# Optimization experiments

Measured on AMD Instinct MI355X. Metric: run time of the kernel, lower is better.

## Reference

```python
import jax, jax.numpy as jnp
import numpy as np

DIM = 768
HEADS = 12
HEAD_DIM = DIM // HEADS
EPS_ATTN = 1e-6
LN_EPS = 1e-5


def _piece_weight():
    # BlockDistanceConv with num_patches_per_side=16, patch_group_size=16 -> 4x4 blocks
    bps = 4
    centers = np.array([[i + 0.5, j + 0.5] for i in range(bps) for j in range(bps)], dtype=np.float32)
    d = np.linalg.norm(centers[:, None, :] - centers[None, :, :], axis=-1)
    mat = np.cos(d / d.max() * np.pi / 4.0)  # 'cos' transform
    mat = mat / mat.sum(axis=0, keepdims=True)
    return jnp.asarray(mat, dtype=jnp.float32)  # [16, 16], out = W @ x over piece channels


def setup_inputs() -> dict:
    key = jax.random.key(0)
    ks = jax.random.split(key, 4)
    B, N, W, C = 128, 16, 16, DIM
    x = jax.random.normal(ks[0], (B, N, W, C), dtype=jnp.float32)
    ln_gamma = jnp.ones((C,), dtype=jnp.float32)
    ln_beta = jnp.zeros((C,), dtype=jnp.float32)
    w_qkv = jax.random.normal(ks[1], (C, 3 * C), dtype=jnp.float32) * (C ** -0.5)
    w_out = jax.random.normal(ks[2], (C, C), dtype=jnp.float32) * (C ** -0.5)
    b_out = jnp.zeros((C,), dtype=jnp.float32)
    w_piece = _piece_weight()
    return {"x": x, "ln_gamma": ln_gamma, "ln_beta": ln_beta, "w_qkv": w_qkv,
            "w_out": w_out, "b_out": b_out, "w_piece": w_piece}


def reference(x, ln_gamma, ln_beta, w_qkv, w_out, b_out, w_piece):
    B, N, W, C = x.shape
    H, D = HEADS, HEAD_DIM
    # LayerNorm over channel dim
    mu = jnp.mean(x, axis=-1, keepdims=True)
    var = jnp.mean((x - mu) ** 2, axis=-1, keepdims=True)
    xn = (x - mu) * jax.lax.rsqrt(var + LN_EPS) * ln_gamma + ln_beta
    # qkv projection (no bias)
    qkv = xn @ w_qkv  # [B,N,W,3C]
    q, k, v = jnp.split(qkv, 3, axis=-1)
    # relu kernel feature map
    q = jax.nn.relu(q) + EPS_ATTN
    k = jax.nn.relu(k) + EPS_ATTN
    # split heads: 'b n w (h d) -> b h n w d'
    def heads(t):
        return t.reshape(B, N, W, H, D).transpose(0, 3, 1, 2, 4)
    q, k, v = heads(q), heads(k), heads(v)
    # per-window kv = k^T v  (sum over window positions w)  -> [B,H,N,D,D]
    kv = jnp.einsum('bhnwd,bhnwe->bhnde', k, v)
    # BlockDistanceConv: 1x1 conv mixing over piece dim N with fixed weights
    kv = jnp.einsum('ij,bhjde->bhide', w_piece, kv)
    # out = q @ kv  -> [B,H,N,W,D]
    out = jnp.einsum('bhnwd,bhnde->bhnwe', q, kv)
    # merge heads: 'b h n w d -> b n w (h d)'
    out = out.transpose(0, 2, 3, 1, 4).reshape(B, N, W, H * D)
    # output projection (dropout is identity in eval)
    return out @ w_out + b_out
```

## Files before the change

### kernel.cpp

```cpp
#include <hip/hip_runtime.h>

#define DIM 768
#define HEADS 12
#define TOK 32768

typedef unsigned short ushort_t;
typedef __attribute__((ext_vector_type(8))) short short8v;
typedef __attribute__((ext_vector_type(4))) float f32x4;
typedef __attribute__((ext_vector_type(4))) unsigned short us4;

__device__ __forceinline__ ushort_t f2bf(float x) {
  union { float f; unsigned u; } c; c.f = x;
  unsigned r = (c.u + 0x7FFFu + ((c.u >> 16) & 1u)) >> 16;
  return (ushort_t)r;
}

__device__ __forceinline__ void gload_lds16(const void* g, void* l) {
  __builtin_amdgcn_global_load_lds((const __attribute__((address_space(1))) void*)g,
                                   (__attribute__((address_space(3))) void*)l, 16, 0, 0);
}

__global__ __launch_bounds__(256) void ln_kernel(const float* __restrict__ x,
                                                 const float* __restrict__ g,
                                                 const float* __restrict__ be,
                                                 ushort_t* __restrict__ xn) {
  int t = blockIdx.x;
  int tid = threadIdx.x;
  const float* row = x + (size_t)t * DIM;
  float v0 = row[tid], v1 = row[tid + 256], v2 = row[tid + 512];
  float s  = v0 + v1 + v2;
  float sq = v0 * v0 + v1 * v1 + v2 * v2;
  #pragma unroll
  for (int off = 32; off; off >>= 1) {
    s  += __shfl_down(s, off);
    sq += __shfl_down(sq, off);
  }
  __shared__ float ls[4], lq[4];
  int wid = tid >> 6, lane = tid & 63;
  if (lane == 0) { ls[wid] = s; lq[wid] = sq; }
  __syncthreads();
  s  = ls[0] + ls[1] + ls[2] + ls[3];
  sq = lq[0] + lq[1] + lq[2] + lq[3];
  float mu  = s * (1.0f / DIM);
  float var = sq * (1.0f / DIM) - mu * mu;
  float rs  = rsqrtf(var + 1e-5f);
  ushort_t* orow = xn + (size_t)t * DIM;
  orow[tid]       = f2bf((v0 - mu) * rs * g[tid]       + be[tid]);
  orow[tid + 256] = f2bf((v1 - mu) * rs * g[tid + 256] + be[tid + 256]);
  orow[tid + 512] = f2bf((v2 - mu) * rs * g[tid + 512] + be[tid + 512]);
}

__global__ __launch_bounds__(256) void convT(const float* __restrict__ src,
                                             ushort_t* __restrict__ dst, int R, int Ccol) {
  __shared__ float tile[32][33];
  int c0 = blockIdx.x * 32, r0 = blockIdx.y * 32;
  int tx = threadIdx.x & 31, ty = threadIdx.x >> 5;
  #pragma unroll
  for (int i = 0; i < 32; i += 8)
    tile[ty + i][tx] = src[(size_t)(r0 + ty + i) * Ccol + c0 + tx];
  __syncthreads();
  #pragma unroll
  for (int i = 0; i < 32; i += 8)
    dst[(size_t)(c0 + ty + i) * R + r0 + tx] = f2bf(tile[tx][ty + i]);
}

template <int MODE>
__global__ __launch_bounds__(256) void gemm_ring(const ushort_t* __restrict__ A,
                                                 const ushort_t* __restrict__ Bt,
                                                 ushort_t* __restrict__ qbf,
                                                 ushort_t* __restrict__ kbf,
                                                 ushort_t* __restrict__ vTbf,
                                                 const float* __restrict__ bias,
                                                 float* __restrict__ C) {
  const int K = DIM, Kb = DIM * 2;
  const int N = (MODE == 0) ? 3 * DIM : DIM;
  const int nbn = N / 128;
  const int NT = K / 32;
  __shared__ __align__(16) char lds[4 * 16384];

  int bid = blockIdx.x;
  int qd = gridDim.x >> 3;
  int wid = (bid & 7) * qd + (bid >> 3);
  int bm = wid / nbn, bn = wid % nbn;
  int row0 = bm * 128, col0 = bn * 128;
  int t = threadIdx.x;
  int lane = t & 63, wave = t >> 6;
  int wr = wave >> 1, wc = wave & 1;

  const char* Ag = (const char*)(A + (size_t)row0 * K);
  const char* Bg = (const char*)(Bt + (size_t)col0 * K);

  int o0 = t * 16;
  int o1 = 4096 + t * 16;
  int r0s = o0 >> 6, r1s = o1 >> 6;
  int sb0 = (o0 & 63) ^ ((r0s & 3) << 4);
  int sb1 = (o1 & 63) ^ ((r1s & 3) << 4);
  size_t ga0 = (size_t)r0s * Kb + sb0;
  size_t ga1 = (size_t)r1s * Kb + sb1;

  int fr = lane & 15, fkb = (lane >> 4) << 4;
  int sw = fkb ^ ((fr & 3) << 4);
  int aoff = (wr * 64 + fr) * 64 + sw;
  int boff = (wc * 64 + fr) * 64 + sw;

  #define STAGE(tile, slot)                                            \
    do {                                                               \
      char* sb = lds + ((slot) << 14);                                 \
      gload_lds16(Ag + ga0 + (tile) * 64, sb + o0);                    \
      gload_lds16(Ag + ga1 + (tile) * 64, sb + o1);                    \
      gload_lds16(Bg + ga0 + (tile) * 64, sb + 8192 + o0);             \
      gload_lds16(Bg + ga1 + (tile) * 64, sb + 8192 + o1);             \
    } while (0)

  STAGE(0, 0);
  STAGE(1, 1);

  f32x4 acc[4][4] = {};
  #pragma unroll 2
  for (int kt = 0; kt < NT; ++kt) {
    if (kt + 2 < NT) STAGE(kt + 2, (kt + 2) & 3);
    if (kt < NT - 1) asm volatile("s_waitcnt vmcnt(4)" ::: "memory");
    else             asm volatile("s_waitcnt vmcnt(0)" ::: "memory");
    __builtin_amdgcn_s_barrier();
    const char* As = lds + ((kt & 3) << 14);
    const char* Bs = As + 8192;
    short8v a[4], b[4];
    #pragma unroll
    for (int m = 0; m < 4; ++m) a[m] = *(const short8v*)(As + aoff + m * 1024);
    #pragma unroll
    for (int n = 0; n < 4; ++n) b[n] = *(const short8v*)(Bs + boff + n * 1024);
    __builtin_amdgcn_s_setprio(1);
    #pragma unroll
    for (int m = 0; m < 4; ++m)
      #pragma unroll
      for (int n = 0; n < 4; ++n)
        acc[m][n] = __builtin_amdgcn_mfma_f32_16x16x32_bf16(a[m], b[n], acc[m][n], 0, 0, 0);
    __builtin_amdgcn_s_setprio(0);
  }
  #undef STAGE

  int rbase = row0 + wr * 64 + ((lane >> 4) << 2);
  int cbase = col0 + wc * 64 + fr;
  if constexpr (MODE == 0) {
    #pragma unroll
    for (int m = 0; m < 4; ++m) {
      int r0r = rbase + m * 16;
      #pragma unroll
      for (int n = 0; n < 4; ++n) {
        int c = cbase + n * 16;
        if (c < DIM) {
          #pragma unroll
          for (int j = 0; j < 4; ++j)
            qbf[(size_t)(r0r + j) * DIM + c] = f2bf(fmaxf(acc[m][n][j], 0.0f) + 1e-6f);
        } else if (c < 2 * DIM) {
          #pragma unroll
          for (int j = 0; j < 4; ++j)
            kbf[(size_t)(r0r + j) * DIM + (c - DIM)] = f2bf(fmaxf(acc[m][n][j], 0.0f) + 1e-6f);
        } else {
          int ch = c - 2 * DIM;
          int hh = ch >> 6, e = ch & 63;
          int bb = r0r >> 8, rr = r0r & 255;
          us4 pk;
          #pragma unroll
          for (int j = 0; j < 4; ++j) pk[j] = f2bf(acc[m][n][j]);
          *(us4*)&vTbf[((((size_t)bb * HEADS + hh) * 64 + e) << 8) + rr] = pk;
        }
      }
    }
  } else {
    #pragma unroll
    for (int m = 0; m < 4; ++m) {
      #pragma unroll
      for (int n = 0; n < 4; ++n) {
        int c = cbase + n * 16;
        float bz = bias[c];
        #pragma unroll
        for (int j = 0; j < 4; ++j)
          C[(size_t)(rbase + m * 16 + j) * N + c] = acc[m][n][j] + bz;
      }
    }
  }
}

__global__ __launch_bounds__(512) void attn_fused(const ushort_t* __restrict__ qbf,
                                                  const ushort_t* __restrict__ kbf,
                                                  const ushort_t* __restrict__ vTbf,
                                                  const float* __restrict__ wp,
                                                  ushort_t* __restrict__ attnO) {
  __shared__ __align__(16) char lds[65536];
  int bh = blockIdx.x;
  int b = bh / HEADS, h = bh % HEADS;
  int t = threadIdx.x;
  int lane = t & 63, wave = t >> 6;
  int wr = wave >> 2, wc = wave & 3;
  int fr = lane & 15, fkb = (lane >> 4) << 4;

  const char* qg = (const char*)(qbf + ((size_t)b * 256) * DIM + h * 64);
  const char* kg = (const char*)(kbf + ((size_t)b * 256) * DIM + h * 64);
  const char* vg = (const char*)(vTbf + ((size_t)bh << 14));

  for (int q4 = 0; q4 < 4; ++q4) {
    #pragma unroll
    for (int is = 0; is < 4; ++is) {
      int o = is * 8192 + t * 16;
      int r = o >> 7;
      int byt = (o & 127) ^ ((r & 7) << 4);
      gload_lds16(kg + (size_t)r * (DIM * 2) + byt, lds + o);
    }
    {
      int o = t * 16;
      int r = o >> 7;
      int byt = (o & 127) ^ ((r & 7) << 4);
      gload_lds16(qg + (size_t)(q4 * 64 + r) * (DIM * 2) + byt, lds + 32768 + o);
    }
    __syncthreads();
    f32x4 accA[2][4] = {};
    {
      short8v af[2][2], bfv[4][2];
      #pragma unroll
      for (int mt = 0; mt < 2; ++mt)
        #pragma unroll
        for (int ks = 0; ks < 2; ++ks) {
          int r = wr * 32 + mt * 16 + fr;
          int kb = ks * 64 + fkb;
          af[mt][ks] = *(const short8v*)(lds + 32768 + r * 128 + (kb ^ ((r & 7) << 4)));
        }
      #pragma unroll
      for (int nt = 0; nt < 4; ++nt)
        #pragma unroll
        for (int ks = 0; ks < 2; ++ks) {
          int c = wc * 64 + nt * 16 + fr;
          int kb = ks * 64 + fkb;
          bfv[nt][ks] = *(const short8v*)(lds + c * 128 + (kb ^ ((c & 7) << 4)));
        }
      #pragma unroll
      for (int mt = 0; mt < 2; ++mt)
        #pragma unroll
        for (int nt = 0; nt < 4; ++nt)
          #pragma unroll
          for (int ks = 0; ks < 2; ++ks)
            accA[mt][nt] = __builtin_amdgcn_mfma_f32_16x16x32_bf16(af[mt][ks], bfv[nt][ks],
                                                                   accA[mt][nt], 0, 0, 0);
    }
    ushort_t sv[2][4][4];
    #pragma unroll
    for (int mt = 0; mt < 2; ++mt)
      #pragma unroll
      for (int nt = 0; nt < 4; ++nt) {
        float wpf = wp[(q4 * 4 + wr * 2 + mt) * 16 + (wc * 4 + nt)];
        #pragma unroll
        for (int j = 0; j < 4; ++j) sv[mt][nt][j] = f2bf(accA[mt][nt][j] * wpf);
      }
    __syncthreads();
    #pragma unroll
    for (int mt = 0; mt < 2; ++mt)
      #pragma unroll
      for (int nt = 0; nt < 4; ++nt)
        #pragma unroll
        for (int j = 0; j < 4; ++j) {
          int rs = wr * 32 + mt * 16 + ((lane >> 4) << 2) + j;
          int cs = wc * 64 + nt * 16 + fr;
          *(ushort_t*)(lds + 32768 + rs * 512 + ((cs * 2) ^ ((rs & 7) << 4))) = sv[mt][nt][j];
        }
    #pragma unroll
    for (int is = 0; is < 4; ++is) {
      int o = is * 8192 + t * 16;
      int e = o >> 9;
      int byt = (o & 511) ^ ((e & 7) << 4);
      gload_lds16(vg + e * 512 + byt, lds + o);
    }
    __syncthreads();
    f32x4 accB[2] = {{0.f,0.f,0.f,0.f},{0.f,0.f,0.f,0.f}};
    #pragma unroll
    for (int ks = 0; ks < 8; ++ks) {
      int kb = ks * 64 + fkb;
      int e = wc * 16 + fr;
      short8v bv = *(const short8v*)(lds + e * 512 + (kb ^ ((e & 7) << 4)));
      #pragma unroll
      for (int mt = 0; mt < 2; ++mt) {
        int r = wr * 32 + mt * 16 + fr;
        short8v av = *(const short8v*)(lds + 32768 + r * 512 + (kb ^ ((r & 7) << 4)));
        accB[mt] = __builtin_amdgcn_mfma_f32_16x16x32_bf16(av, bv, accB[mt], 0, 0, 0);
      }
    }
    #pragma unroll
    for (int mt = 0; mt < 2; ++mt) {
      int row = b * 256 + q4 * 64 + wr * 32 + mt * 16 + ((lane >> 4) << 2);
      int col = h * 64 + wc * 16 + fr;
      #pragma unroll
      for (int j = 0; j < 4; ++j)
        attnO[(size_t)(row + j) * DIM + col] = f2bf(accB[mt][j]);
    }
    __syncthreads();
  }
}

extern "C" void kernel_launch(void* const* d_in, const int* in_sizes, int n_in,
                              void* d_out, int out_size, void* d_ws, size_t ws_size,
                              hipStream_t stream) {
  const float* x    = (const float*)d_in[0];
  const float* g    = (const float*)d_in[1];
  const float* be   = (const float*)d_in[2];
  const float* wqkv = (const float*)d_in[3];
  const float* wout = (const float*)d_in[4];
  const float* bout = (const float*)d_in[5];
  const float* wp   = (const float*)d_in[6];
  float* out = (float*)d_out;

  char* w = (char*)d_ws;
  const size_t SZ = (size_t)TOK * DIM * 2;
  ushort_t* qbf   = (ushort_t*)(w);
  ushort_t* kbf   = (ushort_t*)(w + SZ);
  ushort_t* vTbf  = (ushort_t*)(w + 2 * SZ);
  ushort_t* xn    = (ushort_t*)(w + 3 * SZ);
  ushort_t* wqkvT = (ushort_t*)(w + 4 * SZ);
  ushort_t* woutT = (ushort_t*)(w + 4 * SZ + 3538944);
  ushort_t* attnO = xn;

  dim3 gt1(3 * DIM / 32, DIM / 32);
  convT<<<gt1, 256, 0, stream>>>(wqkv, wqkvT, DIM, 3 * DIM);
  dim3 gt2(DIM / 32, DIM / 32);
  convT<<<gt2, 256, 0, stream>>>(wout, woutT, DIM, DIM);

  ln_kernel<<<TOK, 256, 0, stream>>>(x, g, be, xn);

  gemm_ring<0><<<(TOK / 128) * (3 * DIM / 128), 256, 0, stream>>>(
      xn, wqkvT, qbf, kbf, vTbf, nullptr, nullptr);

  attn_fused<<<128 * HEADS, 512, 0, stream>>>(qbf, kbf, vTbf, wp, attnO);

  gemm_ring<1><<<(TOK / 128) * (DIM / 128), 256, 0, stream>>>(
      attnO, woutT, nullptr, nullptr, nullptr, bout, out);
}
```

Measured before the change: 333.5 us.

## Enlarge GEMM tiles to 256x256 with 8 waves and dynamic LDS

Both projection GEMMs move from 128x128 tiles on 4 waves to 256x256 tiles on 8 waves, each wave computing 128x64 with 8x4 MFMA accumulators. The LDS ring becomes 4 stages of 32KB each (128KB dynamic shared memory), and the vmcnt waits are retuned for 4 loads per stage with two stages in flight. The goal is more reuse of each loaded tile per byte fetched, which cuts global and LDS traffic per FLOP. In exchange, register pressure and LDS use go up, so occupancy falls to roughly one block per CU. The grid also shrinks, especially for the 768-wide output GEMM (384 blocks), which risks poor CU balance.

```diff
diff --git a/kernel.cpp b/kernel.cpp
--- a/kernel.cpp
+++ b/kernel.cpp
@@ -65,73 +65,76 @@
 }
 
 template <int MODE>
-__global__ __launch_bounds__(256) void gemm_ring(const ushort_t* __restrict__ A,
-                                                 const ushort_t* __restrict__ Bt,
-                                                 ushort_t* __restrict__ qbf,
-                                                 ushort_t* __restrict__ kbf,
-                                                 ushort_t* __restrict__ vTbf,
-                                                 const float* __restrict__ bias,
-                                                 float* __restrict__ C) {
+__global__ __launch_bounds__(512, 2) void gemm_big(const ushort_t* __restrict__ A,
+                                                   const ushort_t* __restrict__ Bt,
+                                                   ushort_t* __restrict__ qbf,
+                                                   ushort_t* __restrict__ kbf,
+                                                   ushort_t* __restrict__ vTbf,
+                                                   const float* __restrict__ bias,
+                                                   float* __restrict__ C) {
+  extern __shared__ __align__(16) char lds[];
   const int K = DIM, Kb = DIM * 2;
   const int N = (MODE == 0) ? 3 * DIM : DIM;
-  const int nbn = N / 128;
+  const int nbn = N / 256;
   const int NT = K / 32;
-  __shared__ __align__(16) char lds[4 * 16384];
 
   int bid = blockIdx.x;
   int qd = gridDim.x >> 3;
   int wid = (bid & 7) * qd + (bid >> 3);
   int bm = wid / nbn, bn = wid % nbn;
-  int row0 = bm * 128, col0 = bn * 128;
+  int row0 = bm * 256, col0 = bn * 256;
   int t = threadIdx.x;
   int lane = t & 63, wave = t >> 6;
-  int wr = wave >> 1, wc = wave & 1;
+  int wr = wave >> 2, wcol = wave & 3;
 
   const char* Ag = (const char*)(A + (size_t)row0 * K);
   const char* Bg = (const char*)(Bt + (size_t)col0 * K);
 
-  int o0 = t * 16;
-  int o1 = 4096 + t * 16;
-  int r0s = o0 >> 6, r1s = o1 >> 6;
-  int sb0 = (o0 & 63) ^ ((r0s & 3) << 4);
-  int sb1 = (o1 & 63) ^ ((r1s & 3) << 4);
-  size_t ga0 = (size_t)r0s * Kb + sb0;
-  size_t ga1 = (size_t)r1s * Kb + sb1;
+  int o0 = t * 16, o1 = 8192 + t * 16;
+  int ra0 = o0 >> 6, ra1 = o1 >> 6;
+  int cb0 = (o0 & 63) ^ ((ra0 & 3) << 4);
+  int cb1 = (o1 & 63) ^ ((ra1 & 3) << 4);
+  size_t ga0 = (size_t)ra0 * Kb + cb0;
+  size_t ga1 = (size_t)ra1 * Kb + cb1;
 
   int fr = lane & 15, fkb = (lane >> 4) << 4;
   int sw = fkb ^ ((fr & 3) << 4);
-  int aoff = (wr * 64 + fr) * 64 + sw;
-  int boff = (wc * 64 + fr) * 64 + sw;
+  int aoff = (wr * 128 + fr) * 64 + sw;
+  int boff = 16384 + (wcol * 64 + fr) * 64 + sw;
 
   #define STAGE(tile, slot)                                            \
     do {                                                               \
-      char* sb = lds + ((slot) << 14);                                 \
-      gload_lds16(Ag + ga0 + (tile) * 64, sb + o0);                    \
-      gload_lds16(Ag + ga1 + (tile) * 64, sb + o1);                    \
-      gload_lds16(Bg + ga0 + (tile) * 64, sb + 8192 + o0);             \
-      gload_lds16(Bg + ga1 + (tile) * 64, sb + 8192 + o1);             \
+      char* sb = lds + ((slot) * 32768);                               \
+      size_t kb_ = (size_t)(tile) * 64;                                \
+      gload_lds16(Ag + ga0 + kb_, sb + o0);                            \
+      gload_lds16(Ag + ga1 + kb_, sb + o1);                            \
+      gload_lds16(Bg + ga0 + kb_, sb + 16384 + o0);                    \
+      gload_lds16(Bg + ga1 + kb_, sb + 16384 + o1);                    \
     } while (0)
 
   STAGE(0, 0);
   STAGE(1, 1);
 
-  f32x4 acc[4][4] = {};
-  #pragma unroll 2
+  f32x4 acc[8][4] = {};
   for (int kt = 0; kt < NT; ++kt) {
-    if (kt + 2 < NT) STAGE(kt + 2, (kt + 2) & 3);
-    if (kt < NT - 1) asm volatile("s_waitcnt vmcnt(4)" ::: "memory");
-    else             asm volatile("s_waitcnt vmcnt(0)" ::: "memory");
+    if (kt + 2 < NT) {
+      STAGE(kt + 2, (kt + 2) & 3);
+      asm volatile("s_waitcnt vmcnt(8)" ::: "memory");
+    } else if (kt + 2 == NT) {
+      asm volatile("s_waitcnt vmcnt(4)" ::: "memory");
+    } else {
+      asm volatile("s_waitcnt vmcnt(0)" ::: "memory");
+    }
     __builtin_amdgcn_s_barrier();
-    const char* As = lds + ((kt & 3) << 14);
-    const char* Bs = As + 8192;
-    short8v a[4], b[4];
-    #pragma unroll
-    for (int m = 0; m < 4; ++m) a[m] = *(const short8v*)(As + aoff + m * 1024);
-    #pragma unroll
-    for (int n = 0; n < 4; ++n) b[n] = *(const short8v*)(Bs + boff + n * 1024);
+    const char* As = lds + ((kt & 3) * 32768);
+    short8v a[8], b[4];
+    #pragma unroll
+    for (int m = 0; m < 8; ++m) a[m] = *(const short8v*)(As + aoff + m * 1024);
+    #pragma unroll
+    for (int n = 0; n < 4; ++n) b[n] = *(const short8v*)(As + boff + n * 1024);
     __builtin_amdgcn_s_setprio(1);
     #pragma unroll
-    for (int m = 0; m < 4; ++m)
+    for (int m = 0; m < 8; ++m)
       #pragma unroll
       for (int n = 0; n < 4; ++n)
         acc[m][n] = __builtin_amdgcn_mfma_f32_16x16x32_bf16(a[m], b[n], acc[m][n], 0, 0, 0);
@@ -139,11 +142,11 @@
   }
   #undef STAGE
 
-  int rbase = row0 + wr * 64 + ((lane >> 4) << 2);
-  int cbase = col0 + wc * 64 + fr;
+  int rbase = row0 + wr * 128 + ((lane >> 4) << 2);
+  int cbase = col0 + wcol * 64 + fr;
   if constexpr (MODE == 0) {
     #pragma unroll
-    for (int m = 0; m < 4; ++m) {
+    for (int m = 0; m < 8; ++m) {
       int r0r = rbase + m * 16;
       #pragma unroll
       for (int n = 0; n < 4; ++n) {
@@ -169,7 +172,7 @@
     }
   } else {
     #pragma unroll
-    for (int m = 0; m < 4; ++m) {
+    for (int m = 0; m < 8; ++m) {
       #pragma unroll
       for (int n = 0; n < 4; ++n) {
         int c = cbase + n * 16;
@@ -317,6 +320,11 @@
   ushort_t* woutT = (ushort_t*)(w + 4 * SZ + 3538944);
   ushort_t* attnO = xn;
 
+  (void)hipFuncSetAttribute(reinterpret_cast<const void*>(&gemm_big<0>),
+                            hipFuncAttributeMaxDynamicSharedMemorySize, 131072);
+  (void)hipFuncSetAttribute(reinterpret_cast<const void*>(&gemm_big<1>),
+                            hipFuncAttributeMaxDynamicSharedMemorySize, 131072);
+
   dim3 gt1(3 * DIM / 32, DIM / 32);
   convT<<<gt1, 256, 0, stream>>>(wqkv, wqkvT, DIM, 3 * DIM);
   dim3 gt2(DIM / 32, DIM / 32);
@@ -324,11 +332,11 @@
 
   ln_kernel<<<TOK, 256, 0, stream>>>(x, g, be, xn);
 
-  gemm_ring<0><<<(TOK / 128) * (3 * DIM / 128), 256, 0, stream>>>(
+  gemm_big<0><<<(TOK / 256) * (3 * DIM / 256), 512, 131072, stream>>>(
       xn, wqkvT, qbf, kbf, vTbf, nullptr, nullptr);
 
   attn_fused<<<128 * HEADS, 512, 0, stream>>>(qbf, kbf, vTbf, wp, attnO);
 
-  gemm_ring<1><<<(TOK / 128) * (DIM / 128), 256, 0, stream>>>(
+  gemm_big<1><<<(TOK / 256) * (DIM / 256), 512, 131072, stream>>>(
       attnO, woutT, nullptr, nullptr, nullptr, bout, out);
 }
```

Result: faster. 321.3 us (-3.7%).
